# Kernel optimization log

Measured on AMD Instinct MI355X. Metric: run time of the kernel, lower is better.

Reference implementation:

```python
import jax, jax.numpy as jnp
import numpy as np

BATCH, SEQ = 2, 2048
HID = 2048          # hidden_size
INTER = 4096        # intermediate_size
STATE = 16          # ssm_state_size
RANK = 128          # time_step_rank
K = 4               # conv_kernel


def setup_inputs() -> dict:
    key = jax.random.key(0)
    ks = jax.random.split(key, 8)
    s = 0.02
    return {
        "hidden_states": jax.random.normal(ks[0], (BATCH, SEQ, HID), jnp.float32),
        "in_proj_w": jax.random.normal(ks[1], (2 * INTER, HID), jnp.float32) * s,
        "conv_w": jax.random.normal(ks[2], (INTER, 1, K), jnp.float32) * s,   # depthwise (O, I/g=1, K)
        "conv_b": jnp.zeros((INTER,), jnp.float32),
        "x_proj_w": jax.random.normal(ks[3], (RANK + 2 * STATE, INTER), jnp.float32) * s,
        "dt_proj_w": jax.random.normal(ks[4], (INTER, RANK), jnp.float32) * s,
        "dt_proj_b": jax.random.normal(ks[5], (INTER,), jnp.float32) * s,
        "A_log": jnp.log(jnp.broadcast_to(jnp.arange(1, STATE + 1, dtype=jnp.float32), (INTER, STATE))),
        "D": jnp.ones((INTER,), jnp.float32),
        "out_proj_w": jax.random.normal(ks[6], (HID, INTER), jnp.float32) * s,
    }


def reference(hidden_states, in_proj_w, conv_w, conv_b, x_proj_w,
              dt_proj_w, dt_proj_b, A_log, D, out_proj_w):
    B, L, _ = hidden_states.shape
    # in_proj -> (B, L, 2*INTER), split into u (SSM input) and gate
    proj = jnp.einsum('blh,ph->blp', hidden_states, in_proj_w)
    u, gate = jnp.split(proj, 2, axis=-1)                       # (B, L, INTER) each
    # depthwise causal conv1d on channel-major layout (B, INTER, L)
    uc = jnp.swapaxes(u, 1, 2)
    conv = jax.lax.conv_general_dilated(
        uc, conv_w, window_strides=(1,), padding=[(K - 1, 0)],
        dimension_numbers=('NCH', 'OIH', 'NCH'), feature_group_count=INTER)
    u = jax.nn.silu(conv + conv_b[None, :, None])               # (B, INTER, L)
    # x_proj: dt-rank + B + C, computed in fp32 like the original
    ssm_p = jnp.einsum('bdl,pd->blp', u, x_proj_w).astype(jnp.float32)
    dt_r, Bm, Cm = jnp.split(ssm_p, [RANK, RANK + STATE], axis=-1)  # (B,L,RANK),(B,L,N),(B,L,N)
    dt = jax.nn.softplus(jnp.einsum('blr,dr->bld', dt_r, dt_proj_w) + dt_proj_b)  # (B, L, INTER)
    A = -jnp.exp(A_log)                                         # (INTER, STATE)

    def step(state, xs):
        dt_t, B_t, C_t, u_t = xs                                # (B,D),(B,N),(B,N),(B,D)
        dA = jnp.exp(dt_t[:, :, None] * A[None])                # (B, D, N)
        state = dA * state + (dt_t * u_t)[:, :, None] * B_t[:, None, :]
        y = jnp.einsum('bdn,bn->bd', state, C_t)
        return state, y

    xs = (jnp.swapaxes(dt, 0, 1),        # (L, B, D)
          jnp.swapaxes(Bm, 0, 1),        # (L, B, N)
          jnp.swapaxes(Cm, 0, 1),        # (L, B, N)
          jnp.moveaxis(u, 2, 0))         # (L, B, D)
    init = jnp.zeros((B, INTER, STATE), jnp.float32)
    _, ys = jax.lax.scan(step, init, xs)                        # (L, B, D)

    y = jnp.moveaxis(ys, 0, 1) + jnp.swapaxes(u, 1, 2) * D[None, None, :]  # skip connection
    y = y * jax.nn.silu(gate)
    return jnp.einsum('bld,hd->blh', y, out_proj_w)             # (B, L, HID)
```

## Files before the change

### kernel.cpp

```cpp
#include <hip/hip_runtime.h>

typedef unsigned int u32;
typedef unsigned short u16;
typedef float f32x4 __attribute__((ext_vector_type(4)));
typedef u16 us4 __attribute__((ext_vector_type(4)));
typedef u16 us8 __attribute__((ext_vector_type(8)));
typedef __bf16 bf16x8 __attribute__((ext_vector_type(8)));

__device__ __forceinline__ u16 f2bf(float f) {
  u32 u = __builtin_bit_cast(u32, f);
  u += 0x7fffu + ((u >> 16) & 1u);
  return (u16)(u >> 16);
}
__device__ __forceinline__ float bf2f(u16 h) {
  u32 u = ((u32)h) << 16;
  return __builtin_bit_cast(float, u);
}
__device__ __forceinline__ void async16(const void* g, void* l) {
  __builtin_amdgcn_global_load_lds((const __attribute__((address_space(1))) void*)g,
                                   (__attribute__((address_space(3))) void*)l, 16, 0, 0);
}

template <int ACT, bool SPLITK = false>
__global__ __launch_bounds__(256) void gemm_bt(const u16* __restrict__ A,
                                               const u16* __restrict__ B,
                                               void* __restrict__ Cv,
                                               const float* __restrict__ bias,
                                               int K, int ldc) {
  __shared__ __align__(16) u16 As[128 * 64];
  __shared__ __align__(16) u16 Bs[128 * 64];
  const int tid = threadIdx.x;
  const int lane = tid & 63;
  const int wave = tid >> 6;
  const int lm = lane & 15;
  const int quad = lane >> 4;
  const int wm = (wave >> 1) << 6;
  const int wn = (wave & 1) << 6;
  const long rowBase = (long)blockIdx.y << 7;
  const long colBase = (long)blockIdx.x << 7;

  int kStart = 0, kEnd = K;
  if constexpr (SPLITK) {
    int kn = K / gridDim.z;
    kStart = blockIdx.z * kn;
    kEnd = kStart + kn;
  }

  const int rr = tid >> 3;
  const int qg = (tid & 7) ^ (rr & 7);
  const u16* Ag = A + (rowBase + rr) * (long)K + qg * 8;
  const u16* Bg = B + (colBase + rr) * (long)K + qg * 8;
  u16* Al = As + tid * 8;
  u16* Bl = Bs + tid * 8;

  f32x4 acc[4][4] = {};
  const int l7 = lm & 7;

  for (int k0 = kStart; k0 < kEnd; k0 += 64) {
#pragma unroll
    for (int c = 0; c < 4; ++c) {
      async16(Ag + 32L * c * K + k0, Al + 2048 * c);
      async16(Bg + 32L * c * K + k0, Bl + 2048 * c);
    }
    __syncthreads();
#pragma unroll
    for (int h = 0; h < 2; ++h) {
      const int xa = ((h * 4 + quad) ^ l7) * 8;
      us8 af[4], bfr[4];
#pragma unroll
      for (int i = 0; i < 4; ++i)
        af[i] = *(const us8*)(As + (wm + i * 16 + lm) * 64 + xa);
#pragma unroll
      for (int i = 0; i < 4; ++i)
        bfr[i] = *(const us8*)(Bs + (wn + i * 16 + lm) * 64 + xa);
#pragma unroll
      for (int i = 0; i < 4; ++i)
#pragma unroll
        for (int j = 0; j < 4; ++j)
          acc[i][j] = __builtin_amdgcn_mfma_f32_16x16x32_bf16(
              __builtin_bit_cast(bf16x8, af[i]), __builtin_bit_cast(bf16x8, bfr[j]),
              acc[i][j], 0, 0, 0);
    }
    __syncthreads();
  }

  float* Cf = (float*)Cv;
  if constexpr (SPLITK)
    Cf += (size_t)blockIdx.z * ((size_t)gridDim.y * 128 * ldc);

#pragma unroll
  for (int i = 0; i < 4; ++i)
#pragma unroll
    for (int j = 0; j < 4; ++j)
#pragma unroll
      for (int r = 0; r < 4; ++r) {
        long row = rowBase + wm + i * 16 + quad * 4 + r;
        long col = colBase + wn + j * 16 + lm;
        float v = acc[i][j][r];
        if constexpr (ACT == 0) {
          Cf[row * ldc + col] = v;
        } else if constexpr (ACT == 1) {
          ((u16*)Cv)[row * ldc + col] = f2bf(v);
        } else if constexpr (ACT == 2) {
          float s = v / (1.f + __expf(-v));
          ((u16*)Cv)[row * ldc + col] = f2bf(s);
        } else if constexpr (ACT == 3) {
          v += bias[col];
          float sp = (v > 20.f) ? v : log1pf(__expf(v));
          Cf[row * ldc + col] = sp;
        } else if constexpr (ACT == 4) {
          v += bias[col];
          float sp = (v > 20.f) ? v : log1pf(__expf(v));
          ((u16*)Cv)[row * ldc + col] = f2bf(sp);
        } else {
          if (colBase < 4096) {
            ((u16*)Cv)[row * 4096 + col] = f2bf(v);
          } else {
            float s = v / (1.f + __expf(-v));
            ((u16*)(size_t)bias)[row * 4096 + (col - 4096)] = f2bf(s);
          }
        }
      }
}

__device__ __forceinline__ void cvt4(const float* __restrict__ in,
                                     u16* __restrict__ out, int i) {
  f32x4 v = ((const f32x4*)in)[i];
  us4 o;
  o[0] = f2bf(v[0]); o[1] = f2bf(v[1]); o[2] = f2bf(v[2]); o[3] = f2bf(v[3]);
  ((us4*)out)[i] = o;
}
__global__ __launch_bounds__(256) void cvt_all(
    const float* __restrict__ hs, const float* __restrict__ wIn,
    const float* __restrict__ wOut, const float* __restrict__ wDt,
    const float* __restrict__ wX, u16* __restrict__ Xb, u16* __restrict__ Winb,
    u16* __restrict__ Wob, u16* __restrict__ Wdtb, u16* __restrict__ Wxb) {
  int i = blockIdx.x * 256 + threadIdx.x;
  if (i < 2097152) { cvt4(hs, Xb, i); return; }
  i -= 2097152;
  if (i < 4194304) { cvt4(wIn, Winb, i); return; }
  i -= 4194304;
  if (i < 2097152) { cvt4(wOut, Wob, i); return; }
  i -= 2097152;
  if (i < 131072) { cvt4(wDt, Wdtb, i); return; }
  i -= 131072;
  if (i >= 262144) return;
  int row = (i << 2) >> 12;
  us4 o;
  if (row < 160) {
    f32x4 v = ((const f32x4*)wX)[i];
    o[0] = f2bf(v[0]); o[1] = f2bf(v[1]); o[2] = f2bf(v[2]); o[3] = f2bf(v[3]);
  } else {
    o[0] = 0; o[1] = 0; o[2] = 0; o[3] = 0;
  }
  ((us4*)Wxb)[i] = o;
}

__global__ __launch_bounds__(256) void xp_reduce(const float* __restrict__ part,
                                                 float* __restrict__ smp,
                                                 u16* __restrict__ dtrb) {
  int i = blockIdx.x * 256 + threadIdx.x;
  const f32x4* p = (const f32x4*)part;
  f32x4 v = p[i];
  v += p[i + 262144];
  v += p[i + 524288];
  v += p[i + 786432];
  ((f32x4*)smp)[i] = v;
  int e = i << 2;
  int c = e & 255;
  if (c < 128) {
    int t = e >> 8;
    us4 o;
    o[0] = f2bf(v[0]); o[1] = f2bf(v[1]); o[2] = f2bf(v[2]); o[3] = f2bf(v[3]);
    *(us4*)(dtrb + t * 128 + c) = o;
  }
}

__global__ __launch_bounds__(256) void conv_silu(const u16* __restrict__ U,
                                                 const float* __restrict__ cw,
                                                 const float* __restrict__ cb,
                                                 u16* __restrict__ out) {
  int i = blockIdx.x * 256 + threadIdx.x;
  int t = i >> 10;
  int d4 = (i & 1023) << 2;
  int l = t & 2047;
  float w[4][4];
#pragma unroll
  for (int j = 0; j < 4; ++j) {
    f32x4 wv = *(const f32x4*)(cw + (d4 + j) * 4);
    w[j][0] = wv[0]; w[j][1] = wv[1]; w[j][2] = wv[2]; w[j][3] = wv[3];
  }
  float r[4] = {cb[d4], cb[d4 + 1], cb[d4 + 2], cb[d4 + 3]};
#pragma unroll
  for (int k = 0; k < 4; ++k) {
    int ll = l - 3 + k;
    if (ll >= 0) {
      us4 xv = *(const us4*)(U + (size_t)(t - 3 + k) * 4096 + d4);
      r[0] += w[0][k] * bf2f(xv[0]);
      r[1] += w[1][k] * bf2f(xv[1]);
      r[2] += w[2][k] * bf2f(xv[2]);
      r[3] += w[3][k] * bf2f(xv[3]);
    }
  }
  us4 o;
#pragma unroll
  for (int j = 0; j < 4; ++j) {
    float v = r[j];
    float s = v / (1.f + __expf(-v));
    o[j] = f2bf(s);
  }
  *(us4*)(out + (size_t)t * 4096 + d4) = o;
}

__global__ __launch_bounds__(256) void scan_part(
    const u16* __restrict__ dt, const u16* __restrict__ ub,
    const float* __restrict__ ssmp, const float* __restrict__ Alog,
    float* __restrict__ Pout, float* __restrict__ Sout) {
  const int tid = threadIdx.x;
  const int chunk = blockIdx.x, dgrp = blockIdx.y, b = blockIdx.z;
  const int d = (dgrp << 8) + tid;
  float A[16];
#pragma unroll
  for (int q = 0; q < 4; ++q) {
    f32x4 v = *(const f32x4*)(Alog + d * 16 + q * 4);
    A[q * 4 + 0] = -__expf(v[0]);
    A[q * 4 + 1] = -__expf(v[1]);
    A[q * 4 + 2] = -__expf(v[2]);
    A[q * 4 + 3] = -__expf(v[3]);
  }
  bool fastl = true;
#pragma unroll
  for (int n = 1; n < 16; ++n)
    fastl = fastl && (fabsf(A[n] - (n + 1) * A[0]) <= 1e-4f * (float)(n + 1));
  const bool fast = (__ballot(fastl) == ~0ull);

  const int base = b * 2048 + chunk * 128;
  const u16* dtp = dt + (size_t)base * 4096 + d;
  const u16* up = ub + (size_t)base * 4096 + d;
  const float* Bp = ssmp + (size_t)base * 256 + 128;

  float s[16] = {};
  float dtsum = 0.f;
  float cdt[8], cu[8], ndt[8] = {}, nu[8] = {};
#pragma unroll
  for (int j = 0; j < 8; ++j) {
    cdt[j] = bf2f(dtp[j * 4096]);
    cu[j] = bf2f(up[j * 4096]);
  }
  for (int l0 = 0; l0 < 128; l0 += 8) {
    if (l0 + 8 < 128) {
      int o = (l0 + 8) * 4096;
#pragma unroll
      for (int j = 0; j < 8; ++j) {
        ndt[j] = bf2f(dtp[o + j * 4096]);
        nu[j] = bf2f(up[o + j * 4096]);
      }
    }
    if (fast) {
#pragma unroll
      for (int j = 0; j < 8; ++j) {
        float e1 = __expf(cdt[j] * A[0]);
        float x = cdt[j] * cu[j];
        const float* Bl = Bp + (l0 + j) * 256;
        f32x4 B0 = *(const f32x4*)(Bl);
        f32x4 B1 = *(const f32x4*)(Bl + 4);
        f32x4 B2 = *(const f32x4*)(Bl + 8);
        f32x4 B3 = *(const f32x4*)(Bl + 12);
        float p = 1.f;
#pragma unroll
        for (int n = 0; n < 16; ++n) {
          p *= e1;
          float Bn = (n < 4) ? B0[n & 3] : (n < 8) ? B1[n & 3] : (n < 12) ? B2[n & 3] : B3[n & 3];
          s[n] = fmaf(p, s[n], x * Bn);
        }
        dtsum += cdt[j];
      }
    } else {
#pragma unroll
      for (int j = 0; j < 8; ++j) {
        float x = cdt[j] * cu[j];
        const float* Bl = Bp + (l0 + j) * 256;
        f32x4 B0 = *(const f32x4*)(Bl);
        f32x4 B1 = *(const f32x4*)(Bl + 4);
        f32x4 B2 = *(const f32x4*)(Bl + 8);
        f32x4 B3 = *(const f32x4*)(Bl + 12);
#pragma unroll
        for (int n = 0; n < 16; ++n) {
          float e = __expf(cdt[j] * A[n]);
          float Bn = (n < 4) ? B0[n & 3] : (n < 8) ? B1[n & 3] : (n < 12) ? B2[n & 3] : B3[n & 3];
          s[n] = fmaf(e, s[n], x * Bn);
        }
        dtsum += cdt[j];
      }
    }
#pragma unroll
    for (int j = 0; j < 8; ++j) { cdt[j] = ndt[j]; cu[j] = nu[j]; }
  }
  size_t o = ((size_t)(b * 16 + chunk) * 16) * 4096 + d;
#pragma unroll
  for (int n = 0; n < 16; ++n) {
    Pout[o + (size_t)n * 4096] = __expf(dtsum * A[n]);
    Sout[o + (size_t)n * 4096] = s[n];
  }
}

__global__ __launch_bounds__(256) void scan_y(
    const u16* __restrict__ dt, const u16* __restrict__ ub,
    const float* __restrict__ ssmp, const u16* __restrict__ gs,
    const float* __restrict__ Alog, const float* __restrict__ Dv,
    const float* __restrict__ Pin, const float* __restrict__ Sin,
    u16* __restrict__ yb) {
  const int tid = threadIdx.x;
  const int chunk = blockIdx.x, dgrp = blockIdx.y, b = blockIdx.z;
  const int d = (dgrp << 8) + tid;
  float A[16];
#pragma unroll
  for (int q = 0; q < 4; ++q) {
    f32x4 v = *(const f32x4*)(Alog + d * 16 + q * 4);
    A[q * 4 + 0] = -__expf(v[0]);
    A[q * 4 + 1] = -__expf(v[1]);
    A[q * 4 + 2] = -__expf(v[2]);
    A[q * 4 + 3] = -__expf(v[3]);
  }
  bool fastl = true;
#pragma unroll
  for (int n = 1; n < 16; ++n)
    fastl = fastl && (fabsf(A[n] - (n + 1) * A[0]) <= 1e-4f * (float)(n + 1));
  const bool fast = (__ballot(fastl) == ~0ull);
  const float Dd = Dv[d];

  const int base = b * 2048 + chunk * 128;
  const u16* dtp = dt + (size_t)base * 4096 + d;
  const u16* up = ub + (size_t)base * 4096 + d;
  const u16* gp = gs + (size_t)base * 4096 + d;
  const float* Bp = ssmp + (size_t)base * 256 + 128;
  u16* yo = yb + (size_t)base * 4096 + d;

  float s[16] = {};
  {
    for (int k = 0; k < chunk; ++k) {
      size_t o = ((size_t)(b * 16 + k) * 16) * 4096 + d;
#pragma unroll
      for (int n = 0; n < 16; ++n) {
        float P = Pin[o + (size_t)n * 4096];
        float S = Sin[o + (size_t)n * 4096];
        s[n] = fmaf(P, s[n], S);
      }
    }
  }

  float cdt[8], cu[8], cg[8], ndt[8] = {}, nu[8] = {}, ng[8] = {};
#pragma unroll
  for (int j = 0; j < 8; ++j) {
    cdt[j] = bf2f(dtp[j * 4096]);
    cu[j] = bf2f(up[j * 4096]);
    cg[j] = bf2f(gp[j * 4096]);
  }
  for (int l0 = 0; l0 < 128; l0 += 8) {
    if (l0 + 8 < 128) {
      int o = (l0 + 8) * 4096;
#pragma unroll
      for (int j = 0; j < 8; ++j) {
        ndt[j] = bf2f(dtp[o + j * 4096]);
        nu[j] = bf2f(up[o + j * 4096]);
        ng[j] = bf2f(gp[o + j * 4096]);
      }
    }
    if (fast) {
#pragma unroll
      for (int j = 0; j < 8; ++j) {
        float e1 = __expf(cdt[j] * A[0]);
        float x = cdt[j] * cu[j];
        const float* Bl = Bp + (l0 + j) * 256;
        f32x4 B0 = *(const f32x4*)(Bl);
        f32x4 B1 = *(const f32x4*)(Bl + 4);
        f32x4 B2 = *(const f32x4*)(Bl + 8);
        f32x4 B3 = *(const f32x4*)(Bl + 12);
        f32x4 C0 = *(const f32x4*)(Bl + 16);
        f32x4 C1 = *(const f32x4*)(Bl + 20);
        f32x4 C2 = *(const f32x4*)(Bl + 24);
        f32x4 C3 = *(const f32x4*)(Bl + 28);
        float p = 1.f;
        float y0 = 0.f, y1 = 0.f, y2 = 0.f, y3 = 0.f;
#pragma unroll
        for (int n = 0; n < 16; ++n) {
          p *= e1;
          float Bn = (n < 4) ? B0[n & 3] : (n < 8) ? B1[n & 3] : (n < 12) ? B2[n & 3] : B3[n & 3];
          float Cn = (n < 4) ? C0[n & 3] : (n < 8) ? C1[n & 3] : (n < 12) ? C2[n & 3] : C3[n & 3];
          s[n] = fmaf(p, s[n], x * Bn);
          if (n < 4) y0 = fmaf(s[n], Cn, y0);
          else if (n < 8) y1 = fmaf(s[n], Cn, y1);
          else if (n < 12) y2 = fmaf(s[n], Cn, y2);
          else y3 = fmaf(s[n], Cn, y3);
        }
        float y = (y0 + y1) + (y2 + y3);
        yo[(l0 + j) * 4096] = f2bf((y + cu[j] * Dd) * cg[j]);
      }
    } else {
#pragma unroll
      for (int j = 0; j < 8; ++j) {
        float x = cdt[j] * cu[j];
        const float* Bl = Bp + (l0 + j) * 256;
        f32x4 B0 = *(const f32x4*)(Bl);
        f32x4 B1 = *(const f32x4*)(Bl + 4);
        f32x4 B2 = *(const f32x4*)(Bl + 8);
        f32x4 B3 = *(const f32x4*)(Bl + 12);
        f32x4 C0 = *(const f32x4*)(Bl + 16);
        f32x4 C1 = *(const f32x4*)(Bl + 20);
        f32x4 C2 = *(const f32x4*)(Bl + 24);
        f32x4 C3 = *(const f32x4*)(Bl + 28);
        float y0 = 0.f, y1 = 0.f, y2 = 0.f, y3 = 0.f;
#pragma unroll
        for (int n = 0; n < 16; ++n) {
          float e = __expf(cdt[j] * A[n]);
          float Bn = (n < 4) ? B0[n & 3] : (n < 8) ? B1[n & 3] : (n < 12) ? B2[n & 3] : B3[n & 3];
          float Cn = (n < 4) ? C0[n & 3] : (n < 8) ? C1[n & 3] : (n < 12) ? C2[n & 3] : C3[n & 3];
          s[n] = fmaf(e, s[n], x * Bn);
          if (n < 4) y0 = fmaf(s[n], Cn, y0);
          else if (n < 8) y1 = fmaf(s[n], Cn, y1);
          else if (n < 12) y2 = fmaf(s[n], Cn, y2);
          else y3 = fmaf(s[n], Cn, y3);
        }
        float y = (y0 + y1) + (y2 + y3);
        yo[(l0 + j) * 4096] = f2bf((y + cu[j] * Dd) * cg[j]);
      }
    }
#pragma unroll
    for (int j = 0; j < 8; ++j) { cdt[j] = ndt[j]; cu[j] = nu[j]; cg[j] = ng[j]; }
  }
}

extern "C" void kernel_launch(void* const* d_in, const int* in_sizes, int n_in,
                              void* d_out, int out_size, void* d_ws,
                              size_t ws_size, hipStream_t stream) {
  (void)in_sizes; (void)n_in; (void)out_size; (void)ws_size;
  const float* hs = (const float*)d_in[0];
  const float* wIn = (const float*)d_in[1];
  const float* cw = (const float*)d_in[2];
  const float* cb = (const float*)d_in[3];
  const float* wX = (const float*)d_in[4];
  const float* wDt = (const float*)d_in[5];
  const float* bDt = (const float*)d_in[6];
  const float* Alog = (const float*)d_in[7];
  const float* Dv = (const float*)d_in[8];
  const float* wOut = (const float*)d_in[9];

  const size_t MB = 1ull << 20;
  char* w = (char*)d_ws;
  u16* Xb = (u16*)(w + 0 * MB);
  u16* Winb = (u16*)(w + 16 * MB);
  u16* Pu = (u16*)(w + 48 * MB);
  u16* Dtb = (u16*)(w + 0 * MB);
  u16* Yb = (u16*)(w + 64 * MB);
  u16* Ub = (u16*)(w + 96 * MB);
  u16* Wxb = (u16*)(w + 128 * MB);
  float* Smp = (float*)(w + 130 * MB);
  u16* Dtrb = (u16*)(w + 134 * MB);
  u16* Wdtb = (u16*)(w + 135 * MB);
  u16* Wob = (u16*)(w + 136 * MB);
  float* Pchk = (float*)(w + 152 * MB);
  float* Schk = (float*)(w + 160 * MB);
  float* Xpart = (float*)(w + 168 * MB);
  u16* Pg = (u16*)d_out;

  cvt_all<<<34304, 256, 0, stream>>>(hs, wIn, wOut, wDt, wX, Xb, Winb, Wob, Wdtb, Wxb);
  gemm_bt<5><<<dim3(64, 32), 256, 0, stream>>>(Xb, Winb, Pu, (const float*)Pg, 2048, 4096);
  conv_silu<<<16384, 256, 0, stream>>>(Pu, cw, cb, Ub);
  gemm_bt<0, true><<<dim3(2, 32, 4), 256, 0, stream>>>(Ub, Wxb, Xpart, nullptr, 4096, 256);
  xp_reduce<<<1024, 256, 0, stream>>>(Xpart, Smp, Dtrb);
  gemm_bt<4><<<dim3(32, 32), 256, 0, stream>>>(Dtrb, Wdtb, Dtb, bDt, 128, 4096);
  scan_part<<<dim3(16, 16, 2), 256, 0, stream>>>(Dtb, Ub, Smp, Alog, Pchk, Schk);
  scan_y<<<dim3(16, 16, 2), 256, 0, stream>>>(Dtb, Ub, Smp, Pg, Alog, Dv, Pchk, Schk, Yb);
  gemm_bt<0><<<dim3(16, 32), 256, 0, stream>>>(Yb, Wob, (float*)d_out, nullptr, 4096, 2048);
}
```

Before: 667.1 us.

## Switch GEMM to 32x32 MFMA and restructure chunked scan with separate fold kernel

```diff
diff --git a/kernel.cpp b/kernel.cpp
--- a/kernel.cpp
+++ b/kernel.cpp
@@ -3,6 +3,7 @@
 typedef unsigned int u32;
 typedef unsigned short u16;
 typedef float f32x4 __attribute__((ext_vector_type(4)));
+typedef float f32x16 __attribute__((ext_vector_type(16)));
 typedef u16 us4 __attribute__((ext_vector_type(4)));
 typedef u16 us8 __attribute__((ext_vector_type(8)));
 typedef __bf16 bf16x8 __attribute__((ext_vector_type(8)));
@@ -32,8 +33,8 @@
   const int tid = threadIdx.x;
   const int lane = tid & 63;
   const int wave = tid >> 6;
-  const int lm = lane & 15;
-  const int quad = lane >> 4;
+  const int ln = lane & 31;
+  const int hw = lane >> 5;
   const int wm = (wave >> 1) << 6;
   const int wn = (wave & 1) << 6;
   const long rowBase = (long)blockIdx.y << 7;
@@ -53,8 +54,8 @@
   u16* Al = As + tid * 8;
   u16* Bl = Bs + tid * 8;
 
-  f32x4 acc[4][4] = {};
-  const int l7 = lm & 7;
+  f32x16 acc[2][2] = {};
+  const int l7 = ln & 7;
 
   for (int k0 = kStart; k0 < kEnd; k0 += 64) {
 #pragma unroll
@@ -64,20 +65,20 @@
     }
     __syncthreads();
 #pragma unroll
-    for (int h = 0; h < 2; ++h) {
-      const int xa = ((h * 4 + quad) ^ l7) * 8;
-      us8 af[4], bfr[4];
-#pragma unroll
-      for (int i = 0; i < 4; ++i)
-        af[i] = *(const us8*)(As + (wm + i * 16 + lm) * 64 + xa);
-#pragma unroll
-      for (int i = 0; i < 4; ++i)
-        bfr[i] = *(const us8*)(Bs + (wn + i * 16 + lm) * 64 + xa);
-#pragma unroll
-      for (int i = 0; i < 4; ++i)
-#pragma unroll
-        for (int j = 0; j < 4; ++j)
-          acc[i][j] = __builtin_amdgcn_mfma_f32_16x16x32_bf16(
+    for (int s = 0; s < 4; ++s) {
+      const int xa = ((s * 2 + hw) ^ l7) * 8;
+      us8 af[2], bfr[2];
+#pragma unroll
+      for (int i = 0; i < 2; ++i)
+        af[i] = *(const us8*)(As + (wm + i * 32 + ln) * 64 + xa);
+#pragma unroll
+      for (int i = 0; i < 2; ++i)
+        bfr[i] = *(const us8*)(Bs + (wn + i * 32 + ln) * 64 + xa);
+#pragma unroll
+      for (int i = 0; i < 2; ++i)
+#pragma unroll
+        for (int j = 0; j < 2; ++j)
+          acc[i][j] = __builtin_amdgcn_mfma_f32_32x32x16_bf16(
               __builtin_bit_cast(bf16x8, af[i]), __builtin_bit_cast(bf16x8, bfr[j]),
               acc[i][j], 0, 0, 0);
     }
@@ -89,13 +90,13 @@
     Cf += (size_t)blockIdx.z * ((size_t)gridDim.y * 128 * ldc);
 
 #pragma unroll
-  for (int i = 0; i < 4; ++i)
-#pragma unroll
-    for (int j = 0; j < 4; ++j)
-#pragma unroll
-      for (int r = 0; r < 4; ++r) {
-        long row = rowBase + wm + i * 16 + quad * 4 + r;
-        long col = colBase + wn + j * 16 + lm;
+  for (int i = 0; i < 2; ++i)
+#pragma unroll
+    for (int j = 0; j < 2; ++j)
+#pragma unroll
+      for (int r = 0; r < 16; ++r) {
+        long row = rowBase + wm + i * 32 + (r & 3) + 8 * (r >> 2) + 4 * hw;
+        long col = colBase + wn + j * 32 + ln;
         float v = acc[i][j][r];
         if constexpr (ACT == 0) {
           Cf[row * ldc + col] = v;
@@ -215,7 +216,7 @@
 __global__ __launch_bounds__(256) void scan_part(
     const u16* __restrict__ dt, const u16* __restrict__ ub,
     const float* __restrict__ ssmp, const float* __restrict__ Alog,
-    float* __restrict__ Pout, float* __restrict__ Sout) {
+    float* __restrict__ Sout, float* __restrict__ dtsumo) {
   const int tid = threadIdx.x;
   const int chunk = blockIdx.x, dgrp = blockIdx.y, b = blockIdx.z;
   const int d = (dgrp << 8) + tid;
@@ -234,7 +235,7 @@
     fastl = fastl && (fabsf(A[n] - (n + 1) * A[0]) <= 1e-4f * (float)(n + 1));
   const bool fast = (__ballot(fastl) == ~0ull);
 
-  const int base = b * 2048 + chunk * 128;
+  const int base = b * 2048 + chunk * 64;
   const u16* dtp = dt + (size_t)base * 4096 + d;
   const u16* up = ub + (size_t)base * 4096 + d;
   const float* Bp = ssmp + (size_t)base * 256 + 128;
@@ -247,8 +248,8 @@
     cdt[j] = bf2f(dtp[j * 4096]);
     cu[j] = bf2f(up[j * 4096]);
   }
-  for (int l0 = 0; l0 < 128; l0 += 8) {
-    if (l0 + 8 < 128) {
+  for (int l0 = 0; l0 < 64; l0 += 8) {
+    if (l0 + 8 < 64) {
       int o = (l0 + 8) * 4096;
 #pragma unroll
       for (int j = 0; j < 8; ++j) {
@@ -296,11 +297,25 @@
 #pragma unroll
     for (int j = 0; j < 8; ++j) { cdt[j] = ndt[j]; cu[j] = nu[j]; }
   }
-  size_t o = ((size_t)(b * 16 + chunk) * 16) * 4096 + d;
-#pragma unroll
-  for (int n = 0; n < 16; ++n) {
-    Pout[o + (size_t)n * 4096] = __expf(dtsum * A[n]);
-    Sout[o + (size_t)n * 4096] = s[n];
+  size_t o = ((size_t)(b * 32 + chunk) * 16) * 4096 + d;
+#pragma unroll
+  for (int n = 0; n < 16; ++n) Sout[o + (size_t)n * 4096] = s[n];
+  dtsumo[(size_t)(b * 32 + chunk) * 4096 + d] = dtsum;
+}
+
+__global__ __launch_bounds__(256) void scan_fold(
+    const float* __restrict__ Sin, const float* __restrict__ dtsum,
+    const float* __restrict__ Alog, float* __restrict__ Sinit) {
+  const int tid = threadIdx.x;
+  const int n = blockIdx.x, dgrp = blockIdx.y, b = blockIdx.z;
+  const int d = (dgrp << 8) + tid;
+  const float A = -__expf(Alog[d * 16 + n]);
+  float run = 0.f;
+  for (int c = 0; c < 32; ++c) {
+    size_t o = ((size_t)(b * 32 + c) * 16 + n) * 4096 + d;
+    Sinit[o] = run;
+    float P = __expf(dtsum[(size_t)(b * 32 + c) * 4096 + d] * A);
+    run = fmaf(P, run, Sin[o]);
   }
 }
 
@@ -308,8 +323,7 @@
     const u16* __restrict__ dt, const u16* __restrict__ ub,
     const float* __restrict__ ssmp, const u16* __restrict__ gs,
     const float* __restrict__ Alog, const float* __restrict__ Dv,
-    const float* __restrict__ Pin, const float* __restrict__ Sin,
-    u16* __restrict__ yb) {
+    const float* __restrict__ Sinit, u16* __restrict__ yb) {
   const int tid = threadIdx.x;
   const int chunk = blockIdx.x, dgrp = blockIdx.y, b = blockIdx.z;
   const int d = (dgrp << 8) + tid;
@@ -329,24 +343,18 @@
   const bool fast = (__ballot(fastl) == ~0ull);
   const float Dd = Dv[d];
 
-  const int base = b * 2048 + chunk * 128;
+  const int base = b * 2048 + chunk * 64;
   const u16* dtp = dt + (size_t)base * 4096 + d;
   const u16* up = ub + (size_t)base * 4096 + d;
   const u16* gp = gs + (size_t)base * 4096 + d;
   const float* Bp = ssmp + (size_t)base * 256 + 128;
   u16* yo = yb + (size_t)base * 4096 + d;
 
-  float s[16] = {};
+  float s[16];
   {
-    for (int k = 0; k < chunk; ++k) {
-      size_t o = ((size_t)(b * 16 + k) * 16) * 4096 + d;
-#pragma unroll
-      for (int n = 0; n < 16; ++n) {
-        float P = Pin[o + (size_t)n * 4096];
-        float S = Sin[o + (size_t)n * 4096];
-        s[n] = fmaf(P, s[n], S);
-      }
-    }
+    size_t o = ((size_t)(b * 32 + chunk) * 16) * 4096 + d;
+#pragma unroll
+    for (int n = 0; n < 16; ++n) s[n] = Sinit[o + (size_t)n * 4096];
   }
 
   float cdt[8], cu[8], cg[8], ndt[8] = {}, nu[8] = {}, ng[8] = {};
@@ -356,8 +364,8 @@
     cu[j] = bf2f(up[j * 4096]);
     cg[j] = bf2f(gp[j * 4096]);
   }
-  for (int l0 = 0; l0 < 128; l0 += 8) {
-    if (l0 + 8 < 128) {
+  for (int l0 = 0; l0 < 64; l0 += 8) {
+    if (l0 + 8 < 64) {
       int o = (l0 + 8) * 4096;
 #pragma unroll
       for (int j = 0; j < 8; ++j) {
@@ -458,9 +466,10 @@
   u16* Dtrb = (u16*)(w + 134 * MB);
   u16* Wdtb = (u16*)(w + 135 * MB);
   u16* Wob = (u16*)(w + 136 * MB);
-  float* Pchk = (float*)(w + 152 * MB);
-  float* Schk = (float*)(w + 160 * MB);
-  float* Xpart = (float*)(w + 168 * MB);
+  float* Schk = (float*)(w + 152 * MB);
+  float* Xpart = (float*)(w + 152 * MB);
+  float* Sinit = (float*)(w + 168 * MB);
+  float* Dtsum = (float*)(w + 184 * MB);
   u16* Pg = (u16*)d_out;
 
   cvt_all<<<34304, 256, 0, stream>>>(hs, wIn, wOut, wDt, wX, Xb, Winb, Wob, Wdtb, Wxb);
@@ -469,7 +478,8 @@
   gemm_bt<0, true><<<dim3(2, 32, 4), 256, 0, stream>>>(Ub, Wxb, Xpart, nullptr, 4096, 256);
   xp_reduce<<<1024, 256, 0, stream>>>(Xpart, Smp, Dtrb);
   gemm_bt<4><<<dim3(32, 32), 256, 0, stream>>>(Dtrb, Wdtb, Dtb, bDt, 128, 4096);
-  scan_part<<<dim3(16, 16, 2), 256, 0, stream>>>(Dtb, Ub, Smp, Alog, Pchk, Schk);
-  scan_y<<<dim3(16, 16, 2), 256, 0, stream>>>(Dtb, Ub, Smp, Pg, Alog, Dv, Pchk, Schk, Yb);
+  scan_part<<<dim3(32, 16, 2), 256, 0, stream>>>(Dtb, Ub, Smp, Alog, Schk, Dtsum);
+  scan_fold<<<dim3(16, 16, 2), 256, 0, stream>>>(Schk, Dtsum, Alog, Sinit);
+  scan_y<<<dim3(32, 16, 2), 256, 0, stream>>>(Dtb, Ub, Smp, Pg, Alog, Dv, Sinit, Yb);
   gemm_bt<0><<<dim3(16, 32), 256, 0, stream>>>(Yb, Wob, (float*)d_out, nullptr, 4096, 2048);
 }
```

Result: faster. 647.7 us (-2.9%).
